# Performance work log

Hardware: AMD Instinct MI355X
Metric: run time of the kernel (lower is better)

Reference implementation:

```python
import jax, jax.numpy as jnp
import numpy as np

B, N, E, D, H = 8, 5000, 160000, 64, 128  # batch, nodes, edges, gnn hidden, head hidden


def _w(key, shape, scale=0.05):
    return jax.random.normal(key, shape, jnp.float32) * scale


def setup_inputs() -> dict:
    key = jax.random.key(0)
    ks = jax.random.split(key, 24)
    inp = {
        "x": jax.random.normal(ks[0], (B, N), jnp.float32),
        "edges": jax.random.randint(ks[1], (E, 2), 0, N, dtype=jnp.int32),
        "emb": _w(ks[2], (N, D)),
        # conv1: prepare FFN (2 layers, no bias, elu), update FFN (2 layers, bias)
        "c1_pw1": _w(ks[3], (D, D)), "c1_pw2": _w(ks[4], (D, D)),
        "c1_uw1": _w(ks[5], (2 * D, D)), "c1_ub1": jnp.zeros((D,), jnp.float32),
        "c1_uw2": _w(ks[6], (D, D)), "c1_ub2": jnp.zeros((D,), jnp.float32),
        # conv2
        "c2_pw1": _w(ks[7], (D, D)), "c2_pw2": _w(ks[8], (D, D)),
        "c2_uw1": _w(ks[9], (2 * D, D)), "c2_ub1": jnp.zeros((D,), jnp.float32),
        "c2_uw2": _w(ks[10], (D, D)), "c2_ub2": jnp.zeros((D,), jnp.float32),
        # TARnet prob heads: flatten -> Dense(H, elu) -> Dense(2) (mu, log_sigma)
        "w0a": _w(ks[11], (N * D, H), 0.005), "b0a": jnp.zeros((H,), jnp.float32),
        "w0b": _w(ks[12], (H, 2)), "b0b": jnp.zeros((2,), jnp.float32),
        "w1a": _w(ks[13], (N * D, H), 0.005), "b1a": jnp.zeros((H,), jnp.float32),
        "w1b": _w(ks[14], (H, 2)), "b1b": jnp.zeros((2,), jnp.float32),
    }
    return inp


def _graph_conv(h, edges, pw1, pw2, uw1, ub1, uw2, ub2):
    # h: [B, N, D]; edges: [E, 2] (parent, node)
    parents = jnp.take(h, edges[:, 0], axis=1)            # [B, E, D] gather
    m = jax.nn.elu(parents @ pw1)                          # prepare FFN (no bias)
    m = jax.nn.elu(m @ pw2)
    agg = jnp.zeros_like(h).at[:, edges[:, 1]].add(m)      # unsorted_segment_sum -> [B, N, D]
    hcat = jnp.concatenate([h, agg], axis=-1)              # combination_type='concat'
    u = jax.nn.elu(hcat @ uw1 + ub1)                       # update FFN
    return u @ uw2 + ub2                                   # final_activation=None


def reference(x, edges, emb,
              c1_pw1, c1_pw2, c1_uw1, c1_ub1, c1_uw2, c1_ub2,
              c2_pw1, c2_pw2, c2_uw1, c2_ub1, c2_uw2, c2_ub2,
              w0a, b0a, w0b, b0b, w1a, b1a, w1b, b1b):
    # node features scale learned per-node embeddings -> [B, N, D]
    h = x[:, :, None] * emb[None, :, :]
    h = _graph_conv(h, edges, c1_pw1, c1_pw2, c1_uw1, c1_ub1, c1_uw2, c1_ub2)
    h = _graph_conv(h, edges, c2_pw1, c2_pw2, c2_uw1, c2_ub1, c2_uw2, c2_ub2)
    phi = h.reshape(h.shape[0], -1)                        # flatten [B, N*D]
    y0 = jax.nn.elu(phi @ w0a + b0a) @ w0b + b0b           # [B, 2] (mu, log_sigma)
    y1 = jax.nn.elu(phi @ w1a + b1a) @ w1b + b1b           # [B, 2]
    return jnp.concatenate([y0, y1], axis=1)               # [B, 4]
```

## Files before the change

### kernel.cpp

```cpp
#include <hip/hip_runtime.h>


constexpr int B = 8, N = 5000, E = 160000, D = 64, H = 128;
constexpr int BN = B * N;
constexpr int ND = N * D;
constexpr long BND = (long)BN * D;
constexpr int KC = 320;
constexpr int NIT = KC / 8;
constexpr int XB = ND / KC;

using f32x4 = __attribute__((ext_vector_type(4))) float;

__device__ __forceinline__ float elu_f(float x) {
    return x > 0.0f ? x : __expf(x) - 1.0f;
}

__device__ __forceinline__ void g2lds16(const float* g, float* l) {
    __builtin_amdgcn_global_load_lds(
        (const __attribute__((address_space(1))) void*)g,
        (__attribute__((address_space(3))) void*)l, 16, 0, 0);
}

__global__ __launch_bounds__(256) void k_scan(const int* __restrict__ cnt,
                                              int* __restrict__ offs) {
    __shared__ int part[256];
    int t = threadIdx.x;
    const int CH = 20;
    int base = t * CH;
    int s = 0;
    for (int i = 0; i < CH; ++i) { int idx = base + i; if (idx < N) s += cnt[idx]; }
    part[t] = s;
    __syncthreads();
    for (int off = 1; off < 256; off <<= 1) {
        int add = (t >= off) ? part[t - off] : 0;
        __syncthreads();
        part[t] += add;
        __syncthreads();
    }
    int run = part[t] - s;
    for (int i = 0; i < CH; ++i) {
        int idx = base + i;
        if (idx < N) { offs[idx] = run; run += cnt[idx]; }
    }
    if (t == 255) offs[N] = run;
}

__global__ __launch_bounds__(256) void k_fill(const int* __restrict__ edges,
                                              const int* __restrict__ offs,
                                              int* __restrict__ cursor,
                                              int* __restrict__ elist) {
    int i = blockIdx.x * 256 + threadIdx.x;
    if (i < E) {
        int child = edges[2 * i + 1];
        int pos = offs[child] + atomicAdd(&cursor[child], 1);
        elist[pos] = edges[2 * i];
    }
}

__global__ __launch_bounds__(512) void k_prepare(const float* __restrict__ xsrc,
                                                 const float* __restrict__ emb,
                                                 const int* __restrict__ edges,
                                                 int* __restrict__ cnt,
                                                 const float* __restrict__ W1,
                                                 const float* __restrict__ W2,
                                                 float* __restrict__ M) {
    __shared__ float sW1[64 * 64];
    __shared__ float sP[128 * 65];
    int t = threadIdx.x;
    int r0 = blockIdx.x * 128;
    {
        int i = blockIdx.x * 512 + t;
        if (i < E) atomicAdd(&cnt[edges[2 * i + 1]], 1);
    }
    for (int i = t; i < 4096; i += 512) sW1[i] = W1[i];
    for (int i = t; i < 128 * 64; i += 512) {
        int r = i >> 6, c = i & 63;
        int row = r0 + r;
        float v = 0.0f;
        if (row < BN) {
            int n = row % N;
            v = xsrc[row] * emb[n * 64 + c];
        }
        sP[r * 65 + c] = v;
    }
    __syncthreads();

    int cg = t & 15, rg = t >> 4;
    float acc[4][4] = {};
    #pragma unroll 4
    for (int k = 0; k < 64; ++k) {
        float a[4];
        #pragma unroll
        for (int i = 0; i < 4; ++i) a[i] = sP[(rg * 4 + i) * 65 + k];
        float4 bb = *reinterpret_cast<const float4*>(&sW1[k * 64 + cg * 4]);
        #pragma unroll
        for (int i = 0; i < 4; ++i) {
            acc[i][0] += a[i] * bb.x; acc[i][1] += a[i] * bb.y;
            acc[i][2] += a[i] * bb.z; acc[i][3] += a[i] * bb.w;
        }
    }
    __syncthreads();
    #pragma unroll
    for (int i = 0; i < 4; ++i)
        #pragma unroll
        for (int j = 0; j < 4; ++j)
            sP[(rg * 4 + i) * 65 + cg * 4 + j] = elu_f(acc[i][j]);
    __syncthreads();

    float acc2[4][4] = {};
    #pragma unroll 4
    for (int k = 0; k < 64; ++k) {
        float a[4];
        #pragma unroll
        for (int i = 0; i < 4; ++i) a[i] = sP[(rg * 4 + i) * 65 + k];
        float4 bb = *reinterpret_cast<const float4*>(&W2[k * 64 + cg * 4]);
        #pragma unroll
        for (int i = 0; i < 4; ++i) {
            acc2[i][0] += a[i] * bb.x; acc2[i][1] += a[i] * bb.y;
            acc2[i][2] += a[i] * bb.z; acc2[i][3] += a[i] * bb.w;
        }
    }
    #pragma unroll
    for (int i = 0; i < 4; ++i) {
        int row = r0 + rg * 4 + i;
        if (row < BN) {
            int b = row / N;
            int n = row - b * N;
            float4 o = make_float4(elu_f(acc2[i][0]), elu_f(acc2[i][1]),
                                   elu_f(acc2[i][2]), elu_f(acc2[i][3]));
            *reinterpret_cast<float4*>(&M[((long)n * 8 + b) * 64 + cg * 4]) = o;
        }
    }
}

template <int PREP>
__global__ __launch_bounds__(512, 8) void k_conv(const float* __restrict__ h,
                                                 const float* __restrict__ xsrc,
                                                 const float* __restrict__ emb,
                                                 const float* __restrict__ M,
                                                 const int* __restrict__ offs,
                                                 const int* __restrict__ elist,
                                                 const float* __restrict__ W1u,
                                                 const float* __restrict__ b1u,
                                                 const float* __restrict__ W2u,
                                                 const float* __restrict__ b2u,
                                                 float* __restrict__ hout,
                                                 const float* __restrict__ W1p,
                                                 const float* __restrict__ W2p,
                                                 float* __restrict__ Mout) {
    __shared__ float sP[64 * 129];
    int t = threadIdx.x;
    int n0 = blockIdx.x * 8;

    #pragma unroll
    for (int q = 0; q < 2; ++q) {
        int s = t + q * 512;
        int lr = s >> 4, c4 = s & 15;
        int nl = lr >> 3, b = lr & 7;
        long grow = (long)b * N + (n0 + nl);
        float4 v;
        if (PREP) {
            float xv = xsrc[grow];
            float4 ev = *reinterpret_cast<const float4*>(
                &emb[(long)(n0 + nl) * 64 + c4 * 4]);
            v = make_float4(xv * ev.x, xv * ev.y, xv * ev.z, xv * ev.w);
        } else {
            v = *reinterpret_cast<const float4*>(&h[grow * 64 + c4 * 4]);
        }
        int base = lr * 129 + c4 * 4;
        sP[base + 0] = v.x; sP[base + 1] = v.y;
        sP[base + 2] = v.z; sP[base + 3] = v.w;
    }
    {
        int wv = t >> 6, l = t & 63;
        int n = n0 + wv;
        int e0 = __builtin_amdgcn_readfirstlane(offs[n]);
        int e1 = __builtin_amdgcn_readfirstlane(offs[n + 1]);
        float4 a1 = make_float4(0.f, 0.f, 0.f, 0.f);
        float4 a2 = make_float4(0.f, 0.f, 0.f, 0.f);
        float4 a3 = make_float4(0.f, 0.f, 0.f, 0.f);
        float4 a4 = make_float4(0.f, 0.f, 0.f, 0.f);
        int e = e0;
        for (; e + 1 < e1; e += 2) {
            int p1 = elist[e], p2 = elist[e + 1];
            const float4* q1 = reinterpret_cast<const float4*>(M + (long)p1 * 512);
            const float4* q2 = reinterpret_cast<const float4*>(M + (long)p2 * 512);
            float4 v1 = q1[l], v2 = q1[64 + l];
            float4 v3 = q2[l], v4 = q2[64 + l];
            a1.x += v1.x; a1.y += v1.y; a1.z += v1.z; a1.w += v1.w;
            a2.x += v2.x; a2.y += v2.y; a2.z += v2.z; a2.w += v2.w;
            a3.x += v3.x; a3.y += v3.y; a3.z += v3.z; a3.w += v3.w;
            a4.x += v4.x; a4.y += v4.y; a4.z += v4.z; a4.w += v4.w;
        }
        if (e < e1) {
            int p = elist[e];
            const float4* q = reinterpret_cast<const float4*>(M + (long)p * 512);
            float4 v1 = q[l], v2 = q[64 + l];
            a1.x += v1.x; a1.y += v1.y; a1.z += v1.z; a1.w += v1.w;
            a2.x += v2.x; a2.y += v2.y; a2.z += v2.z; a2.w += v2.w;
        }
        a1.x += a3.x; a1.y += a3.y; a1.z += a3.z; a1.w += a3.w;
        a2.x += a4.x; a2.y += a4.y; a2.z += a4.z; a2.w += a4.w;
        int c4 = l & 15, br = l >> 4;
        int base1 = (wv * 8 + br) * 129 + 64 + c4 * 4;
        int base2 = (wv * 8 + 4 + br) * 129 + 64 + c4 * 4;
        sP[base1 + 0] = a1.x; sP[base1 + 1] = a1.y;
        sP[base1 + 2] = a1.z; sP[base1 + 3] = a1.w;
        sP[base2 + 0] = a2.x; sP[base2 + 1] = a2.y;
        sP[base2 + 2] = a2.z; sP[base2 + 3] = a2.w;
    }
    __syncthreads();

    int cg = t & 15, rg = t >> 4;
    float acc[2][4] = {};
    #pragma unroll 4
    for (int k = 0; k < 128; ++k) {
        float a0 = sP[(rg * 2 + 0) * 129 + k];
        float a1 = sP[(rg * 2 + 1) * 129 + k];
        float4 bb = *reinterpret_cast<const float4*>(&W1u[k * 64 + cg * 4]);
        acc[0][0] += a0 * bb.x; acc[0][1] += a0 * bb.y; acc[0][2] += a0 * bb.z; acc[0][3] += a0 * bb.w;
        acc[1][0] += a1 * bb.x; acc[1][1] += a1 * bb.y; acc[1][2] += a1 * bb.z; acc[1][3] += a1 * bb.w;
    }
    float4 bv1 = *reinterpret_cast<const float4*>(&b1u[cg * 4]);
    __syncthreads();
    #pragma unroll
    for (int i = 0; i < 2; ++i) {
        int base = (rg * 2 + i) * 129 + cg * 4;
        sP[base + 0] = elu_f(acc[i][0] + bv1.x);
        sP[base + 1] = elu_f(acc[i][1] + bv1.y);
        sP[base + 2] = elu_f(acc[i][2] + bv1.z);
        sP[base + 3] = elu_f(acc[i][3] + bv1.w);
    }
    __syncthreads();

    float acc2[2][4] = {};
    #pragma unroll 4
    for (int k = 0; k < 64; ++k) {
        float a0 = sP[(rg * 2 + 0) * 129 + k];
        float a1 = sP[(rg * 2 + 1) * 129 + k];
        float4 bb = *reinterpret_cast<const float4*>(&W2u[k * 64 + cg * 4]);
        acc2[0][0] += a0 * bb.x; acc2[0][1] += a0 * bb.y; acc2[0][2] += a0 * bb.z; acc2[0][3] += a0 * bb.w;
        acc2[1][0] += a1 * bb.x; acc2[1][1] += a1 * bb.y; acc2[1][2] += a1 * bb.z; acc2[1][3] += a1 * bb.w;
    }
    float4 bv2 = *reinterpret_cast<const float4*>(&b2u[cg * 4]);
    #pragma unroll
    for (int i = 0; i < 2; ++i) {
        int lr = rg * 2 + i;
        int nl = lr >> 3, b = lr & 7;
        float4 o = make_float4(acc2[i][0] + bv2.x, acc2[i][1] + bv2.y,
                               acc2[i][2] + bv2.z, acc2[i][3] + bv2.w);
        *reinterpret_cast<float4*>(
            &hout[((long)b * N + (n0 + nl)) * 64 + cg * 4]) = o;
        if (PREP) {
            int base = lr * 129 + 64 + cg * 4;
            sP[base + 0] = o.x; sP[base + 1] = o.y;
            sP[base + 2] = o.z; sP[base + 3] = o.w;
        }
    }

    if (PREP) {
        __syncthreads();
        float acc3[2][4] = {};
        #pragma unroll 4
        for (int k = 0; k < 64; ++k) {
            float a0 = sP[(rg * 2 + 0) * 129 + 64 + k];
            float a1 = sP[(rg * 2 + 1) * 129 + 64 + k];
            float4 bb = *reinterpret_cast<const float4*>(&W1p[k * 64 + cg * 4]);
            acc3[0][0] += a0 * bb.x; acc3[0][1] += a0 * bb.y; acc3[0][2] += a0 * bb.z; acc3[0][3] += a0 * bb.w;
            acc3[1][0] += a1 * bb.x; acc3[1][1] += a1 * bb.y; acc3[1][2] += a1 * bb.z; acc3[1][3] += a1 * bb.w;
        }
        #pragma unroll
        for (int i = 0; i < 2; ++i) {
            int base = (rg * 2 + i) * 129 + cg * 4;
            sP[base + 0] = elu_f(acc3[i][0]);
            sP[base + 1] = elu_f(acc3[i][1]);
            sP[base + 2] = elu_f(acc3[i][2]);
            sP[base + 3] = elu_f(acc3[i][3]);
        }
        __syncthreads();
        float acc4[2][4] = {};
        #pragma unroll 4
        for (int k = 0; k < 64; ++k) {
            float a0 = sP[(rg * 2 + 0) * 129 + k];
            float a1 = sP[(rg * 2 + 1) * 129 + k];
            float4 bb = *reinterpret_cast<const float4*>(&W2p[k * 64 + cg * 4]);
            acc4[0][0] += a0 * bb.x; acc4[0][1] += a0 * bb.y; acc4[0][2] += a0 * bb.z; acc4[0][3] += a0 * bb.w;
            acc4[1][0] += a1 * bb.x; acc4[1][1] += a1 * bb.y; acc4[1][2] += a1 * bb.z; acc4[1][3] += a1 * bb.w;
        }
        #pragma unroll
        for (int i = 0; i < 2; ++i) {
            int lr = rg * 2 + i;
            int nl = lr >> 3, b = lr & 7;
            float4 o = make_float4(elu_f(acc4[i][0]), elu_f(acc4[i][1]),
                                   elu_f(acc4[i][2]), elu_f(acc4[i][3]));
            *reinterpret_cast<float4*>(
                &Mout[((long)(n0 + nl) * 8 + b) * 64 + cg * 4]) = o;
        }
    }
}

__global__ __launch_bounds__(256) void k_head(const float* __restrict__ phi,
                                              const float* __restrict__ w0a,
                                              const float* __restrict__ w1a,
                                              float* __restrict__ part) {
    __shared__ float smem[4 * 32 * 33];
    __shared__ __align__(16) float wb[8][1024];
    const float* wa = blockIdx.y ? w1a : w0a;
    int t = threadIdx.x;
    int k0 = blockIdx.x * KC;

    #pragma unroll
    for (int b = 0; b < 8; ++b)
        for (int kk = t; kk < KC; kk += 256)
            smem[b * KC + kk] = phi[(long)b * ND + k0 + kk];
    __syncthreads();

    int w = t >> 6, l = t & 63;
    int h4 = l & 31, kh = l >> 5;
    int kl = w * 2 + kh;
    const float* wp = wa + (long)(k0 + kl) * H + h4 * 4;

    float4 acc[8];
    #pragma unroll
    for (int b = 0; b < 8; ++b) acc[b] = make_float4(0.f, 0.f, 0.f, 0.f);

    unsigned my_off =
        (unsigned)(size_t)(__attribute__((address_space(3))) float*)&wb[0][0]
        + (unsigned)t * 16u;

    const float* wq = wp;
    #pragma unroll
    for (int j = 0; j < 8; ++j) {
        g2lds16(wq, &wb[j][w * 256]);
        wq += 8 * H;
    }

#define STEP(I, CNT, OFF, RE)                                              \
    {                                                                      \
        asm volatile("s_waitcnt vmcnt(" #CNT ")" ::: "memory");            \
        __builtin_amdgcn_sched_barrier(0);                                 \
        f32x4 w4;                                                          \
        asm volatile("ds_read_b128 %0, %1 offset:" #OFF                    \
                     : "=v"(w4) : "v"(my_off));                            \
        float pv[8];                                                       \
        _Pragma("unroll")                                                  \
        for (int b = 0; b < 8; ++b)                                        \
            pv[b] = smem[b * KC + (I) * 8 + kl];                           \
        asm volatile("s_waitcnt lgkmcnt(0)" ::: "memory");                 \
        __builtin_amdgcn_sched_barrier(0);                                 \
        _Pragma("unroll")                                                  \
        for (int b = 0; b < 8; ++b) {                                      \
            acc[b].x += pv[b] * w4.x; acc[b].y += pv[b] * w4.y;            \
            acc[b].z += pv[b] * w4.z; acc[b].w += pv[b] * w4.w;            \
        }                                                                  \
        if (RE) {                                                          \
            g2lds16(wq, &wb[(I) & 7][w * 256]);                            \
            wq += 8 * H;                                                   \
        }                                                                  \
    }

#define ROUND8(BASE, RE)                                                   \
    STEP(BASE + 0, 7, 0,     RE) STEP(BASE + 1, 7, 4096,  RE)              \
    STEP(BASE + 2, 7, 8192,  RE) STEP(BASE + 3, 7, 12288, RE)              \
    STEP(BASE + 4, 7, 16384, RE) STEP(BASE + 5, 7, 20480, RE)              \
    STEP(BASE + 6, 7, 24576, RE) STEP(BASE + 7, 7, 28672, RE)

    ROUND8(0, 1) ROUND8(8, 1) ROUND8(16, 1) ROUND8(24, 1)
    STEP(32, 7, 0,     0) STEP(33, 6, 4096,  0)
    STEP(34, 5, 8192,  0) STEP(35, 4, 12288, 0)
    STEP(36, 3, 16384, 0) STEP(37, 2, 20480, 0)
    STEP(38, 1, 24576, 0) STEP(39, 0, 28672, 0)
#undef ROUND8
#undef STEP

    #pragma unroll
    for (int b = 0; b < 8; ++b) {
        acc[b].x += __shfl_xor(acc[b].x, 32);
        acc[b].y += __shfl_xor(acc[b].y, 32);
        acc[b].z += __shfl_xor(acc[b].z, 32);
        acc[b].w += __shfl_xor(acc[b].w, 32);
    }
    __syncthreads();
    if (kh == 0) {
        int base = (w * 32 + h4) * 33;
        #pragma unroll
        for (int b = 0; b < 8; ++b) {
            smem[base + b * 4 + 0] = acc[b].x;
            smem[base + b * 4 + 1] = acc[b].y;
            smem[base + b * 4 + 2] = acc[b].z;
            smem[base + b * 4 + 3] = acc[b].w;
        }
    }
    __syncthreads();

    int h4r = t & 31, br = t >> 5;
    float s0 = 0.f, s1 = 0.f, s2 = 0.f, s3 = 0.f;
    #pragma unroll
    for (int wv = 0; wv < 4; ++wv) {
        int idx = (wv * 32 + h4r) * 33 + br * 4;
        s0 += smem[idx + 0]; s1 += smem[idx + 1];
        s2 += smem[idx + 2]; s3 += smem[idx + 3];
    }
    float* pb = part + ((long)blockIdx.y * XB + blockIdx.x) * 1024;
    *reinterpret_cast<float4*>(&pb[br * H + h4r * 4]) =
        make_float4(s0, s1, s2, s3);
}

__global__ __launch_bounds__(256) void k_reduce(const float* __restrict__ part,
                                                float* __restrict__ hidden2) {
    int idx = blockIdx.x * 256 + threadIdx.x;
    int c = blockIdx.y;
    int y = idx >> 10, j = idx & 1023;
    const float* p = part + (long)y * XB * 1024 + j;
    int x0 = (XB * c) >> 4, x1 = (XB * (c + 1)) >> 4;
    float s0 = 0.f, s1 = 0.f, s2 = 0.f, s3 = 0.f;
    int x = x0;
    for (; x + 3 < x1; x += 4) {
        s0 += p[(long)(x + 0) * 1024];
        s1 += p[(long)(x + 1) * 1024];
        s2 += p[(long)(x + 2) * 1024];
        s3 += p[(long)(x + 3) * 1024];
    }
    for (; x < x1; ++x) s0 += p[(long)x * 1024];
    hidden2[c * 2048 + idx] = s0 + s1 + s2 + s3;
}

__global__ __launch_bounds__(64) void k_final(const float* __restrict__ hidden2,
                                              const float* __restrict__ b0a,
                                              const float* __restrict__ w0b,
                                              const float* __restrict__ b0b,
                                              const float* __restrict__ b1a,
                                              const float* __restrict__ w1b,
                                              const float* __restrict__ b1b,
                                              float* __restrict__ out) {
    int t = threadIdx.x;
    if (t >= 32) return;
    int head = t >> 4, b = (t >> 1) & 7, j = t & 1;
    int base = head * 1024 + b * H;
    const float* ba = head ? b1a : b0a;
    const float* wb = head ? w1b : w0b;
    const float* bb = head ? b1b : b0b;
    float acc = 0.0f;
    for (int hh = 0; hh < H; ++hh) {
        float hv = 0.0f;
        #pragma unroll
        for (int c = 0; c < 16; ++c) hv += hidden2[c * 2048 + base + hh];
        acc += elu_f(hv + ba[hh]) * wb[hh * 2 + j];
    }
    out[b * 4 + head * 2 + j] = acc + bb[j];
}

extern "C" void kernel_launch(void* const* d_in, const int* in_sizes, int n_in,
                              void* d_out, int out_size, void* d_ws, size_t ws_size,
                              hipStream_t stream) {
    const float* x      = (const float*)d_in[0];
    const int*   edges  = (const int*)d_in[1];
    const float* emb    = (const float*)d_in[2];
    const float* c1_pw1 = (const float*)d_in[3];
    const float* c1_pw2 = (const float*)d_in[4];
    const float* c1_uw1 = (const float*)d_in[5];
    const float* c1_ub1 = (const float*)d_in[6];
    const float* c1_uw2 = (const float*)d_in[7];
    const float* c1_ub2 = (const float*)d_in[8];
    const float* c2_pw1 = (const float*)d_in[9];
    const float* c2_pw2 = (const float*)d_in[10];
    const float* c2_uw1 = (const float*)d_in[11];
    const float* c2_ub1 = (const float*)d_in[12];
    const float* c2_uw2 = (const float*)d_in[13];
    const float* c2_ub2 = (const float*)d_in[14];
    const float* w0a    = (const float*)d_in[15];
    const float* b0a    = (const float*)d_in[16];
    const float* w0b    = (const float*)d_in[17];
    const float* b0b    = (const float*)d_in[18];
    const float* w1a    = (const float*)d_in[19];
    const float* b1a    = (const float*)d_in[20];
    const float* w1b    = (const float*)d_in[21];
    const float* b1b    = (const float*)d_in[22];
    float* out = (float*)d_out;

    float* hA      = (float*)d_ws;
    float* hB      = hA + BND;
    float* Mu      = hB + BND;
    float* M2      = Mu + BND;
    float* hidden2 = M2 + BND;
    int* cnt       = (int*)(hidden2 + 32768);
    int* cursor    = cnt + N;
    int* offs      = cursor + N;
    int* elist     = offs + N + 1;
    float* part    = Mu;

    hipMemsetAsync(cnt, 0, 2 * N * sizeof(int), stream);
    k_prepare<<<(BN + 127) / 128, 512, 0, stream>>>(x, emb, edges, cnt,
                                                    c1_pw1, c1_pw2, Mu);
    k_scan<<<1, 256, 0, stream>>>(cnt, offs);
    k_fill<<<(E + 255) / 256, 256, 0, stream>>>(edges, offs, cursor, elist);
    k_conv<1><<<N / 8, 512, 0, stream>>>(nullptr, x, emb, Mu, offs, elist,
                                         c1_uw1, c1_ub1, c1_uw2, c1_ub2, hB,
                                         c2_pw1, c2_pw2, M2);
    k_conv<0><<<N / 8, 512, 0, stream>>>(hB, nullptr, nullptr, M2, offs, elist,
                                         c2_uw1, c2_ub1, c2_uw2, c2_ub2, hA,
                                         nullptr, nullptr, nullptr);
    k_head<<<dim3(XB, 2), 256, 0, stream>>>(hA, w0a, w1a, part);
    k_reduce<<<dim3(8, 16), 256, 0, stream>>>(part, hidden2);
    k_final<<<1, 64, 0, stream>>>(hidden2, b0a, w0b, b0b, b1a, w1b, b1b, out);
}
```

Before: 655.4 us.

## Merge CSR build and head reduction into cooperative kernels with grid sync

Replaces the memset, edge-count, scan and fill kernels with one cooperative kernel that uses grid-wide syncs between phases, and merges the partial-sum reduce and final head kernels into a second cooperative kernel. Edge counting moves out of k_prepare into the CSR kernel. The aim is to cut kernel launch count and inter-kernel gaps. In exchange it adds grid.sync overhead and puts the serial single-block scan inside a 256-block grid, and cooperative launches can cost more than plain launches.

```diff
diff --git a/kernel.cpp b/kernel.cpp
--- a/kernel.cpp
+++ b/kernel.cpp
@@ -1,4 +1,7 @@
 #include <hip/hip_runtime.h>
+#include <hip/hip_cooperative_groups.h>
+
+namespace cg = cooperative_groups;
 
 
 constexpr int B = 8, N = 5000, E = 160000, D = 64, H = 128;
@@ -21,36 +24,46 @@
         (__attribute__((address_space(3))) void*)l, 16, 0, 0);
 }
 
-__global__ __launch_bounds__(256) void k_scan(const int* __restrict__ cnt,
-                                              int* __restrict__ offs) {
-    __shared__ int part[256];
+__global__ __launch_bounds__(256) void k_csr(const int* __restrict__ edges,
+                                             int* __restrict__ cnt,
+                                             int* __restrict__ cursor,
+                                             int* __restrict__ offs,
+                                             int* __restrict__ elist) {
+    cg::grid_group grid = cg::this_grid();
     int t = threadIdx.x;
-    const int CH = 20;
-    int base = t * CH;
-    int s = 0;
-    for (int i = 0; i < CH; ++i) { int idx = base + i; if (idx < N) s += cnt[idx]; }
-    part[t] = s;
-    __syncthreads();
-    for (int off = 1; off < 256; off <<= 1) {
-        int add = (t >= off) ? part[t - off] : 0;
+    int gtid = blockIdx.x * 256 + t;
+    int GT = gridDim.x * 256;
+
+    for (int i = gtid; i < 2 * N; i += GT) cnt[i] = 0;
+    grid.sync();
+
+    for (int i = gtid; i < E; i += GT) atomicAdd(&cnt[edges[2 * i + 1]], 1);
+    grid.sync();
+
+    if (blockIdx.x == 0) {
+        __shared__ int part[256];
+        const int CH = 20;
+        int base = t * CH;
+        int s = 0;
+        for (int i = 0; i < CH; ++i) { int idx = base + i; if (idx < N) s += cnt[idx]; }
+        part[t] = s;
         __syncthreads();
-        part[t] += add;
-        __syncthreads();
-    }
-    int run = part[t] - s;
-    for (int i = 0; i < CH; ++i) {
-        int idx = base + i;
-        if (idx < N) { offs[idx] = run; run += cnt[idx]; }
-    }
-    if (t == 255) offs[N] = run;
-}
-
-__global__ __launch_bounds__(256) void k_fill(const int* __restrict__ edges,
-                                              const int* __restrict__ offs,
-                                              int* __restrict__ cursor,
-                                              int* __restrict__ elist) {
-    int i = blockIdx.x * 256 + threadIdx.x;
-    if (i < E) {
+        for (int off = 1; off < 256; off <<= 1) {
+            int add = (t >= off) ? part[t - off] : 0;
+            __syncthreads();
+            part[t] += add;
+            __syncthreads();
+        }
+        int run = part[t] - s;
+        for (int i = 0; i < CH; ++i) {
+            int idx = base + i;
+            if (idx < N) { offs[idx] = run; run += cnt[idx]; }
+        }
+        if (t == 255) offs[N] = run;
+    }
+    grid.sync();
+
+    for (int i = gtid; i < E; i += GT) {
         int child = edges[2 * i + 1];
         int pos = offs[child] + atomicAdd(&cursor[child], 1);
         elist[pos] = edges[2 * i];
@@ -59,8 +72,6 @@
 
 __global__ __launch_bounds__(512) void k_prepare(const float* __restrict__ xsrc,
                                                  const float* __restrict__ emb,
-                                                 const int* __restrict__ edges,
-                                                 int* __restrict__ cnt,
                                                  const float* __restrict__ W1,
                                                  const float* __restrict__ W2,
                                                  float* __restrict__ M) {
@@ -68,10 +79,6 @@
     __shared__ float sP[128 * 65];
     int t = threadIdx.x;
     int r0 = blockIdx.x * 128;
-    {
-        int i = blockIdx.x * 512 + t;
-        if (i < E) atomicAdd(&cnt[edges[2 * i + 1]], 1);
-    }
     for (int i = t; i < 4096; i += 512) sW1[i] = W1[i];
     for (int i = t; i < 128 * 64; i += 512) {
         int r = i >> 6, c = i & 63;
@@ -85,14 +92,14 @@
     }
     __syncthreads();
 
-    int cg = t & 15, rg = t >> 4;
+    int cg_ = t & 15, rg = t >> 4;
     float acc[4][4] = {};
     #pragma unroll 4
     for (int k = 0; k < 64; ++k) {
         float a[4];
         #pragma unroll
         for (int i = 0; i < 4; ++i) a[i] = sP[(rg * 4 + i) * 65 + k];
-        float4 bb = *reinterpret_cast<const float4*>(&sW1[k * 64 + cg * 4]);
+        float4 bb = *reinterpret_cast<const float4*>(&sW1[k * 64 + cg_ * 4]);
         #pragma unroll
         for (int i = 0; i < 4; ++i) {
             acc[i][0] += a[i] * bb.x; acc[i][1] += a[i] * bb.y;
@@ -104,7 +111,7 @@
     for (int i = 0; i < 4; ++i)
         #pragma unroll
         for (int j = 0; j < 4; ++j)
-            sP[(rg * 4 + i) * 65 + cg * 4 + j] = elu_f(acc[i][j]);
+            sP[(rg * 4 + i) * 65 + cg_ * 4 + j] = elu_f(acc[i][j]);
     __syncthreads();
 
     float acc2[4][4] = {};
@@ -113,7 +120,7 @@
         float a[4];
         #pragma unroll
         for (int i = 0; i < 4; ++i) a[i] = sP[(rg * 4 + i) * 65 + k];
-        float4 bb = *reinterpret_cast<const float4*>(&W2[k * 64 + cg * 4]);
+        float4 bb = *reinterpret_cast<const float4*>(&W2[k * 64 + cg_ * 4]);
         #pragma unroll
         for (int i = 0; i < 4; ++i) {
             acc2[i][0] += a[i] * bb.x; acc2[i][1] += a[i] * bb.y;
@@ -128,7 +135,7 @@
             int n = row - b * N;
             float4 o = make_float4(elu_f(acc2[i][0]), elu_f(acc2[i][1]),
                                    elu_f(acc2[i][2]), elu_f(acc2[i][3]));
-            *reinterpret_cast<float4*>(&M[((long)n * 8 + b) * 64 + cg * 4]) = o;
+            *reinterpret_cast<float4*>(&M[((long)n * 8 + b) * 64 + cg_ * 4]) = o;
         }
     }
 }
@@ -211,21 +218,21 @@
     }
     __syncthreads();
 
-    int cg = t & 15, rg = t >> 4;
+    int cg_ = t & 15, rg = t >> 4;
     float acc[2][4] = {};
     #pragma unroll 4
     for (int k = 0; k < 128; ++k) {
         float a0 = sP[(rg * 2 + 0) * 129 + k];
         float a1 = sP[(rg * 2 + 1) * 129 + k];
-        float4 bb = *reinterpret_cast<const float4*>(&W1u[k * 64 + cg * 4]);
+        float4 bb = *reinterpret_cast<const float4*>(&W1u[k * 64 + cg_ * 4]);
         acc[0][0] += a0 * bb.x; acc[0][1] += a0 * bb.y; acc[0][2] += a0 * bb.z; acc[0][3] += a0 * bb.w;
         acc[1][0] += a1 * bb.x; acc[1][1] += a1 * bb.y; acc[1][2] += a1 * bb.z; acc[1][3] += a1 * bb.w;
     }
-    float4 bv1 = *reinterpret_cast<const float4*>(&b1u[cg * 4]);
+    float4 bv1 = *reinterpret_cast<const float4*>(&b1u[cg_ * 4]);
     __syncthreads();
     #pragma unroll
     for (int i = 0; i < 2; ++i) {
-        int base = (rg * 2 + i) * 129 + cg * 4;
+        int base = (rg * 2 + i) * 129 + cg_ * 4;
         sP[base + 0] = elu_f(acc[i][0] + bv1.x);
         sP[base + 1] = elu_f(acc[i][1] + bv1.y);
         sP[base + 2] = elu_f(acc[i][2] + bv1.z);
@@ -238,11 +245,11 @@
     for (int k = 0; k < 64; ++k) {
         float a0 = sP[(rg * 2 + 0) * 129 + k];
         float a1 = sP[(rg * 2 + 1) * 129 + k];
-        float4 bb = *reinterpret_cast<const float4*>(&W2u[k * 64 + cg * 4]);
+        float4 bb = *reinterpret_cast<const float4*>(&W2u[k * 64 + cg_ * 4]);
         acc2[0][0] += a0 * bb.x; acc2[0][1] += a0 * bb.y; acc2[0][2] += a0 * bb.z; acc2[0][3] += a0 * bb.w;
         acc2[1][0] += a1 * bb.x; acc2[1][1] += a1 * bb.y; acc2[1][2] += a1 * bb.z; acc2[1][3] += a1 * bb.w;
     }
-    float4 bv2 = *reinterpret_cast<const float4*>(&b2u[cg * 4]);
+    float4 bv2 = *reinterpret_cast<const float4*>(&b2u[cg_ * 4]);
     #pragma unroll
     for (int i = 0; i < 2; ++i) {
         int lr = rg * 2 + i;
@@ -250,9 +257,9 @@
         float4 o = make_float4(acc2[i][0] + bv2.x, acc2[i][1] + bv2.y,
                                acc2[i][2] + bv2.z, acc2[i][3] + bv2.w);
         *reinterpret_cast<float4*>(
-            &hout[((long)b * N + (n0 + nl)) * 64 + cg * 4]) = o;
+            &hout[((long)b * N + (n0 + nl)) * 64 + cg_ * 4]) = o;
         if (PREP) {
-            int base = lr * 129 + 64 + cg * 4;
+            int base = lr * 129 + 64 + cg_ * 4;
             sP[base + 0] = o.x; sP[base + 1] = o.y;
             sP[base + 2] = o.z; sP[base + 3] = o.w;
         }
@@ -265,13 +272,13 @@
         for (int k = 0; k < 64; ++k) {
             float a0 = sP[(rg * 2 + 0) * 129 + 64 + k];
             float a1 = sP[(rg * 2 + 1) * 129 + 64 + k];
-            float4 bb = *reinterpret_cast<const float4*>(&W1p[k * 64 + cg * 4]);
+            float4 bb = *reinterpret_cast<const float4*>(&W1p[k * 64 + cg_ * 4]);
             acc3[0][0] += a0 * bb.x; acc3[0][1] += a0 * bb.y; acc3[0][2] += a0 * bb.z; acc3[0][3] += a0 * bb.w;
             acc3[1][0] += a1 * bb.x; acc3[1][1] += a1 * bb.y; acc3[1][2] += a1 * bb.z; acc3[1][3] += a1 * bb.w;
         }
         #pragma unroll
         for (int i = 0; i < 2; ++i) {
-            int base = (rg * 2 + i) * 129 + cg * 4;
+            int base = (rg * 2 + i) * 129 + cg_ * 4;
             sP[base + 0] = elu_f(acc3[i][0]);
             sP[base + 1] = elu_f(acc3[i][1]);
             sP[base + 2] = elu_f(acc3[i][2]);
@@ -283,7 +290,7 @@
         for (int k = 0; k < 64; ++k) {
             float a0 = sP[(rg * 2 + 0) * 129 + k];
             float a1 = sP[(rg * 2 + 1) * 129 + k];
-            float4 bb = *reinterpret_cast<const float4*>(&W2p[k * 64 + cg * 4]);
+            float4 bb = *reinterpret_cast<const float4*>(&W2p[k * 64 + cg_ * 4]);
             acc4[0][0] += a0 * bb.x; acc4[0][1] += a0 * bb.y; acc4[0][2] += a0 * bb.z; acc4[0][3] += a0 * bb.w;
             acc4[1][0] += a1 * bb.x; acc4[1][1] += a1 * bb.y; acc4[1][2] += a1 * bb.z; acc4[1][3] += a1 * bb.w;
         }
@@ -294,7 +301,7 @@
             float4 o = make_float4(elu_f(acc4[i][0]), elu_f(acc4[i][1]),
                                    elu_f(acc4[i][2]), elu_f(acc4[i][3]));
             *reinterpret_cast<float4*>(
-                &Mout[((long)(n0 + nl) * 8 + b) * 64 + cg * 4]) = o;
+                &Mout[((long)(n0 + nl) * 8 + b) * 64 + cg_ * 4]) = o;
         }
     }
 }
@@ -406,48 +413,51 @@
         make_float4(s0, s1, s2, s3);
 }
 
-__global__ __launch_bounds__(256) void k_reduce(const float* __restrict__ part,
-                                                float* __restrict__ hidden2) {
-    int idx = blockIdx.x * 256 + threadIdx.x;
-    int c = blockIdx.y;
-    int y = idx >> 10, j = idx & 1023;
-    const float* p = part + (long)y * XB * 1024 + j;
-    int x0 = (XB * c) >> 4, x1 = (XB * (c + 1)) >> 4;
-    float s0 = 0.f, s1 = 0.f, s2 = 0.f, s3 = 0.f;
-    int x = x0;
-    for (; x + 3 < x1; x += 4) {
-        s0 += p[(long)(x + 0) * 1024];
-        s1 += p[(long)(x + 1) * 1024];
-        s2 += p[(long)(x + 2) * 1024];
-        s3 += p[(long)(x + 3) * 1024];
-    }
-    for (; x < x1; ++x) s0 += p[(long)x * 1024];
-    hidden2[c * 2048 + idx] = s0 + s1 + s2 + s3;
-}
-
-__global__ __launch_bounds__(64) void k_final(const float* __restrict__ hidden2,
-                                              const float* __restrict__ b0a,
-                                              const float* __restrict__ w0b,
-                                              const float* __restrict__ b0b,
-                                              const float* __restrict__ b1a,
-                                              const float* __restrict__ w1b,
-                                              const float* __restrict__ b1b,
-                                              float* __restrict__ out) {
-    int t = threadIdx.x;
-    if (t >= 32) return;
-    int head = t >> 4, b = (t >> 1) & 7, j = t & 1;
-    int base = head * 1024 + b * H;
-    const float* ba = head ? b1a : b0a;
-    const float* wb = head ? w1b : w0b;
-    const float* bb = head ? b1b : b0b;
-    float acc = 0.0f;
-    for (int hh = 0; hh < H; ++hh) {
-        float hv = 0.0f;
-        #pragma unroll
-        for (int c = 0; c < 16; ++c) hv += hidden2[c * 2048 + base + hh];
-        acc += elu_f(hv + ba[hh]) * wb[hh * 2 + j];
-    }
-    out[b * 4 + head * 2 + j] = acc + bb[j];
+__global__ __launch_bounds__(256) void k_redfin(const float* __restrict__ part,
+                                                float* __restrict__ hidden2,
+                                                const float* __restrict__ b0a,
+                                                const float* __restrict__ w0b,
+                                                const float* __restrict__ b0b,
+                                                const float* __restrict__ b1a,
+                                                const float* __restrict__ w1b,
+                                                const float* __restrict__ b1b,
+                                                float* __restrict__ out) {
+    cg::grid_group grid = cg::this_grid();
+    {
+        int bx = blockIdx.x;
+        int c = bx & 15;
+        int idx = (bx >> 4) * 256 + threadIdx.x;
+        int y = idx >> 10, j = idx & 1023;
+        const float* p = part + (long)y * XB * 1024 + j;
+        int x0 = (XB * c) >> 4, x1 = (XB * (c + 1)) >> 4;
+        float s0 = 0.f, s1 = 0.f, s2 = 0.f, s3 = 0.f;
+        int x = x0;
+        for (; x + 3 < x1; x += 4) {
+            s0 += p[(long)(x + 0) * 1024];
+            s1 += p[(long)(x + 1) * 1024];
+            s2 += p[(long)(x + 2) * 1024];
+            s3 += p[(long)(x + 3) * 1024];
+        }
+        for (; x < x1; ++x) s0 += p[(long)x * 1024];
+        hidden2[c * 2048 + idx] = s0 + s1 + s2 + s3;
+    }
+    grid.sync();
+    if (blockIdx.x == 0 && threadIdx.x < 32) {
+        int t = threadIdx.x;
+        int head = t >> 4, b = (t >> 1) & 7, j = t & 1;
+        int base = head * 1024 + b * H;
+        const float* ba = head ? b1a : b0a;
+        const float* wb2 = head ? w1b : w0b;
+        const float* bb = head ? b1b : b0b;
+        float acc = 0.0f;
+        for (int hh = 0; hh < H; ++hh) {
+            float hv = 0.0f;
+            #pragma unroll
+            for (int c = 0; c < 16; ++c) hv += hidden2[c * 2048 + base + hh];
+            acc += elu_f(hv + ba[hh]) * wb2[hh * 2 + j];
+        }
+        out[b * 4 + head * 2 + j] = acc + bb[j];
+    }
 }
 
 extern "C" void kernel_launch(void* const* d_in, const int* in_sizes, int n_in,
@@ -489,11 +499,13 @@
     int* elist     = offs + N + 1;
     float* part    = Mu;
 
-    hipMemsetAsync(cnt, 0, 2 * N * sizeof(int), stream);
-    k_prepare<<<(BN + 127) / 128, 512, 0, stream>>>(x, emb, edges, cnt,
-                                                    c1_pw1, c1_pw2, Mu);
-    k_scan<<<1, 256, 0, stream>>>(cnt, offs);
-    k_fill<<<(E + 255) / 256, 256, 0, stream>>>(edges, offs, cursor, elist);
+    {
+        void* args[] = {(void*)&edges, (void*)&cnt, (void*)&cursor,
+                        (void*)&offs, (void*)&elist};
+        hipLaunchCooperativeKernel((const void*)k_csr, dim3(256), dim3(256),
+                                   args, 0, stream);
+    }
+    k_prepare<<<(BN + 127) / 128, 512, 0, stream>>>(x, emb, c1_pw1, c1_pw2, Mu);
     k_conv<1><<<N / 8, 512, 0, stream>>>(nullptr, x, emb, Mu, offs, elist,
                                          c1_uw1, c1_ub1, c1_uw2, c1_ub2, hB,
                                          c2_pw1, c2_pw2, M2);
@@ -501,6 +513,11 @@
                                          c2_uw1, c2_ub1, c2_uw2, c2_ub2, hA,
                                          nullptr, nullptr, nullptr);
     k_head<<<dim3(XB, 2), 256, 0, stream>>>(hA, w0a, w1a, part);
-    k_reduce<<<dim3(8, 16), 256, 0, stream>>>(part, hidden2);
-    k_final<<<1, 64, 0, stream>>>(hidden2, b0a, w0b, b0b, b1a, w1b, b1b, out);
-}
+    {
+        void* args[] = {(void*)&part, (void*)&hidden2,
+                        (void*)&b0a, (void*)&w0b, (void*)&b0b,
+                        (void*)&b1a, (void*)&w1b, (void*)&b1b, (void*)&out};
+        hipLaunchCooperativeKernel((const void*)k_redfin, dim3(128), dim3(256),
+                                   args, 0, stream);
+    }
+}
```

Result: slower. 796.8 us (+21.6%).
